# Optimization experiments

Hardware: AMD Instinct MI355X
Metric: run time of the kernel (lower is better)

The kernel has to match this reference:

```python
import jax, jax.numpy as jnp
import numpy as np

B, T, D = 8, 512, 1024
H, DQK, DV = 16, 128, 128  # n_heads, d_qk = emb_dim//h_qk, d_v = emb_dim//h_v


def setup_inputs() -> dict:
    key = jax.random.key(0)
    ks = jax.random.split(key, 8)
    s = 0.02
    return {
        "X": jax.random.normal(ks[0], (B, T, D), jnp.float32),
        "pos_enc_k": jax.random.normal(ks[1], (T, T, DQK), jnp.float32) * s,
        "pos_enc_v": jax.random.normal(ks[2], (T, T, DV), jnp.float32) * s,
        "Wq": jax.random.normal(ks[3], (D, H * DQK), jnp.float32) * s,
        "bq": jnp.zeros((H * DQK,), jnp.float32),
        "Wk": jax.random.normal(ks[4], (D, H * DQK), jnp.float32) * s,
        "bk": jnp.zeros((H * DQK,), jnp.float32),
        "Wv": jax.random.normal(ks[5], (D, H * DV), jnp.float32) * s,
        "bv": jnp.zeros((H * DV,), jnp.float32),
        "Wp": jax.random.normal(ks[6], (H * DV, D), jnp.float32) * s,
        "bp": jnp.zeros((D,), jnp.float32),
    }


def reference(X, pos_enc_k, pos_enc_v, Wq, bq, Wk, bk, Wv, bv, Wp, bp):
    b, t, d = X.shape
    # projections -> (b, h, t, dhead)
    Q = (X @ Wq + bq).reshape(b, t, H, DQK).transpose(0, 2, 1, 3)
    K = (X @ Wk + bk).reshape(b, t, H, DQK).transpose(0, 2, 1, 3)
    V = (X @ Wv + bv).reshape(b, t, H, DV).transpose(0, 2, 1, 3)
    # content attention + relative-position key bias
    att = jnp.einsum("bhqd,bhkd->bhqk", Q, K)
    att = att + jnp.einsum("bhqd,qkd->bhqk", Q, pos_enc_k)
    att = att / jnp.sqrt(jnp.asarray(DQK, X.dtype))
    # causal mask (do_mask=True)
    causal = jnp.tril(jnp.ones((t, t), bool))
    att = jnp.where(causal[None, None], att, jnp.asarray(-jnp.inf, att.dtype))
    att = jax.nn.softmax(att, axis=-1)
    # values + relative-position value correction
    y = jnp.einsum("bhqk,bhkd->bhqd", att, V)
    y = y + jnp.einsum("bhqk,qkd->bhqd", att, pos_enc_v)
    y = y.transpose(0, 2, 1, 3).reshape(b, t, H * DV)
    return y @ Wp + bp
```

## Files before the change

kernel.cpp:

```cpp
#include <hip/hip_runtime.h>
#include <stdint.h>

#define B_  8
#define T_  512
#define D_  1024
#define H_  16
#define DH  128
#define BH  128
#define ND  2048
#define BT  4096

typedef __attribute__((ext_vector_type(8))) short          short8;
typedef __attribute__((ext_vector_type(8))) __bf16         bf16x8;
typedef __attribute__((ext_vector_type(4))) float          f32x4;
typedef __attribute__((ext_vector_type(4))) unsigned short ushort4v;

static __device__ __forceinline__ unsigned short f2bf(float f) {
  unsigned u = __builtin_bit_cast(unsigned, f);
  u += 0x7FFFu + ((u >> 16) & 1u);
  return (unsigned short)(u >> 16);
}
static __device__ __forceinline__ float bf2f(unsigned short h) {
  unsigned u = ((unsigned)h) << 16;
  return __builtin_bit_cast(float, u);
}
static __device__ __forceinline__ f32x4 mfma16(short8 a, short8 b, f32x4 c) {
  return __builtin_amdgcn_mfma_f32_16x16x32_bf16(
      __builtin_bit_cast(bf16x8, a), __builtin_bit_cast(bf16x8, b), c, 0, 0, 0);
}
static __device__ __forceinline__ void gload16(const unsigned short* g, unsigned short* l) {
  __builtin_amdgcn_global_load_lds(
      (const __attribute__((address_space(1))) void*)g,
      (__attribute__((address_space(3))) void*)l, 16, 0, 0);
}

template <int ROWS, int COLS>
static __device__ __forceinline__ void stage_gl2(unsigned short* lds,
                                                 const unsigned short* __restrict__ src,
                                                 long stride, int tid) {
  constexpr int CPR = COLS / 8;
#pragma unroll
  for (int it = 0; it < ROWS * COLS / 8 / 256; ++it) {
    int chunk = tid + it * 256;
    int r = chunk / CPR, c8 = (chunk % CPR) * 8;
    gload16(src + (long)r * stride + c8, lds + chunk * 8);
  }
}

template <int MR, int NR, int LDA, int LDB, int KD>
static __device__ __forceinline__ void mfma_blk(const unsigned short* As,
                                                const unsigned short* Bs,
                                                int a0, int b0, int lrow, int lk8,
                                                f32x4 (*acc)[NR]) {
#pragma unroll
  for (int ks = 0; ks < KD; ks += 32) {
    short8 a[MR], b[NR];
#pragma unroll
    for (int i = 0; i < MR; ++i) a[i] = *(const short8*)&As[(a0 + i * 16 + lrow) * LDA + ks + lk8];
#pragma unroll
    for (int j = 0; j < NR; ++j) b[j] = *(const short8*)&Bs[(b0 + j * 16 + lrow) * LDB + ks + lk8];
#pragma unroll
    for (int i = 0; i < MR; ++i)
#pragma unroll
      for (int j = 0; j < NR; ++j) acc[i][j] = mfma16(a[i], b[j], acc[i][j]);
  }
}

#define IDS4                             \
  const int tid  = threadIdx.x;          \
  const int lane = tid & 63;             \
  const int wid  = tid >> 6;             \
  const int lrow = lane & 15;            \
  const int lk8  = (lane >> 4) * 8;      \
  const int lr4  = (lane >> 4) * 4;      \
  const int wm = wid >> 1, wn = wid & 1;

#define LTS 132
#define LTQ 68

__global__ __launch_bounds__(256) void k_cvt(const float* __restrict__ in,
                                             unsigned short* __restrict__ outp, int n4) {
  int i = blockIdx.x * 256 + threadIdx.x;
  if (i >= n4) return;
  f32x4 v = ((const f32x4*)in)[i];
  ushort4v o;
  o.x = f2bf(v.x); o.y = f2bf(v.y); o.z = f2bf(v.z); o.w = f2bf(v.w);
  ((ushort4v*)outp)[i] = o;
}

__global__ __launch_bounds__(256) void k_transcvt(const float* __restrict__ in,
                                                  unsigned short* __restrict__ outp,
                                                  int R, int C) {
  __shared__ float tile[32][33];
  int c0 = blockIdx.x * 32, r0 = blockIdx.y * 32;
  int tx = threadIdx.x & 31, ty = threadIdx.x >> 5;
#pragma unroll
  for (int i = 0; i < 32; i += 8)
    tile[ty + i][tx] = in[(long)(r0 + ty + i) * C + (c0 + tx)];
  __syncthreads();
#pragma unroll
  for (int i = 0; i < 32; i += 8)
    outp[(long)(c0 + ty + i) * R + (r0 + tx)] = f2bf(tile[tx][ty + i]);
}

__global__ __launch_bounds__(256) void k_vtrans(const unsigned short* __restrict__ vin,
                                                unsigned short* __restrict__ vout) {
  __shared__ unsigned short tile[32][33];
  int bh = blockIdx.z;
  int t0 = blockIdx.x * 32, d0 = blockIdx.y * 32;
  int tx = threadIdx.x & 31, ty = threadIdx.x >> 5;
#pragma unroll
  for (int i = 0; i < 32; i += 8)
    tile[ty + i][tx] = vin[((long)bh * T_ + t0 + ty + i) * DH + (d0 + tx)];
  __syncthreads();
#pragma unroll
  for (int i = 0; i < 32; i += 8)
    vout[((long)bh * DH + (d0 + ty + i)) * T_ + (t0 + tx)] = tile[tx][ty + i];
}

__global__ __launch_bounds__(512, 1) void k_proj8(const unsigned short* __restrict__ Xb,
                                                  const unsigned short* __restrict__ WT,
                                                  const float* __restrict__ bq,
                                                  const float* __restrict__ bk,
                                                  const float* __restrict__ bv,
                                                  unsigned short* __restrict__ Qb,
                                                  unsigned short* __restrict__ Kb,
                                                  unsigned short* __restrict__ Vb) {
  __shared__ unsigned short lds[3 * 24576];
  const int tid  = threadIdx.x;
  const int lane = tid & 63;
  const int wid  = tid >> 6;
  const int wm   = wid >> 2;
  const int wn   = wid & 3;
  const int lrow = lane & 15;
  const int lr4  = (lane >> 4) * 4;

  const int flat = blockIdx.x, xcd = flat & 7, local = flat >> 3;
  const int mt = (xcd & 1) * 16 + (local & 15);
  const int nt = (xcd >> 1) * 6 + (local >> 4);
  const int m0 = mt * 128, n0 = nt * 256;

  const unsigned short* Asrc = Xb + (long)m0 * D_;
  const unsigned short* Bsrc = WT + (long)n0 * D_;

  auto stageA = [&](int t) {
    unsigned short* base = lds + (t % 3) * 24576;
    const unsigned short* as = Asrc + t * 64;
#pragma unroll
    for (int it = 0; it < 2; ++it) {
      int n = tid + it * 512;
      int r = n >> 3, c = (n & 7) ^ (r & 7);
      gload16(as + (long)r * D_ + c * 8, base + n * 8);
    }
  };
  auto stageB = [&](int t) {
    unsigned short* base = lds + (t % 3) * 24576 + 8192;
    const unsigned short* bs = Bsrc + t * 64;
#pragma unroll
    for (int it = 0; it < 4; ++it) {
      int n = tid + it * 512;
      int r = n >> 3, c = (n & 7) ^ (r & 7);
      gload16(bs + (long)r * D_ + c * 8, base + 8192 + n * 8 - 8192);
    }
  };

  stageA(0); stageB(0);
  stageA(1); stageB(1);

  f32x4 acc[4][4] = {};
  for (int t = 0; t < 16; ++t) {
    if (t < 15) asm volatile("s_waitcnt vmcnt(6)" ::: "memory");
    else        asm volatile("s_waitcnt vmcnt(0)" ::: "memory");
    __builtin_amdgcn_sched_barrier(0);
    __builtin_amdgcn_s_barrier();
    __builtin_amdgcn_sched_barrier(0);
    const unsigned short* At = lds + (t % 3) * 24576;
    const unsigned short* Bt = At + 8192;
    {
      short8 a[4], b[4];
#pragma unroll
      for (int i = 0; i < 4; ++i) {
        int ra = wm * 64 + i * 16 + lrow;
        int c = (lane >> 4) ^ (ra & 7);
        a[i] = *(const short8*)&At[ra * 64 + c * 8];
      }
#pragma unroll
      for (int j = 0; j < 4; ++j) {
        int rb = wn * 64 + j * 16 + lrow;
        int c = (lane >> 4) ^ (rb & 7);
        b[j] = *(const short8*)&Bt[rb * 64 + c * 8];
      }
      if (t < 14) stageA(t + 2);
      __builtin_amdgcn_s_setprio(1);
#pragma unroll
      for (int i = 0; i < 4; ++i)
#pragma unroll
        for (int j = 0; j < 4; ++j)
          acc[i][j] = mfma16(a[i], b[j], acc[i][j]);
      __builtin_amdgcn_s_setprio(0);
    }
    __builtin_amdgcn_s_barrier();
    __builtin_amdgcn_sched_barrier(0);
    {
      short8 a[4], b[4];
#pragma unroll
      for (int i = 0; i < 4; ++i) {
        int ra = wm * 64 + i * 16 + lrow;
        int c = (4 + (lane >> 4)) ^ (ra & 7);
        a[i] = *(const short8*)&At[ra * 64 + c * 8];
      }
#pragma unroll
      for (int j = 0; j < 4; ++j) {
        int rb = wn * 64 + j * 16 + lrow;
        int c = (4 + (lane >> 4)) ^ (rb & 7);
        b[j] = *(const short8*)&Bt[rb * 64 + c * 8];
      }
      if (t < 14) stageB(t + 2);
      __builtin_amdgcn_s_setprio(1);
#pragma unroll
      for (int i = 0; i < 4; ++i)
#pragma unroll
        for (int j = 0; j < 4; ++j)
          acc[i][j] = mfma16(a[i], b[j], acc[i][j]);
      __builtin_amdgcn_s_setprio(0);
    }
  }

  const int nb = n0 >> 11;
  const float* biasp = nb == 0 ? bq : (nb == 1 ? bk : bv);
  unsigned short* dst = nb == 0 ? Qb : (nb == 1 ? Kb : Vb);
#pragma unroll
  for (int i = 0; i < 4; ++i)
#pragma unroll
    for (int j = 0; j < 4; ++j) {
      int c = (n0 & 2047) + wn * 64 + j * 16 + lrow;
      int h = c >> 7, dd = c & 127;
      float bias = biasp[c];
#pragma unroll
      for (int r = 0; r < 4; ++r) {
        int m = m0 + wm * 64 + i * 16 + lr4 + r;
        int bb = m >> 9, tt = m & (T_ - 1);
        dst[((long)(bb * H_ + h) * T_ + tt) * DH + dd] = f2bf(acc[i][j][r] + bias);
      }
    }
}

__global__ __launch_bounds__(256) void k_posk(const unsigned short* __restrict__ Qb,
                                              const float* __restrict__ Pk,
                                              unsigned short* __restrict__ att) {
  const int bid = blockIdx.x;
  const int q = (bid & 1) ? (T_ - 1 - (bid >> 1)) : (bid >> 1);
  const int ktiles = (q >> 6) + 1;
  __shared__ unsigned short As[128 * 128];
  __shared__ unsigned short Bs[2][64 * 136];
  IDS4
  stage_gl2<128, 128>(As, Qb + (long)q * DH, (long)T_ * DH, tid);
  f32x4 pv[8];
  const float* psrc = Pk + (long)q * T_ * DH;
  auto loadPk = [&](int kt) {
#pragma unroll
    for (int it = 0; it < 8; ++it) {
      int chunk = tid + it * 256;
      int r = chunk >> 5, c4 = (chunk & 31) * 4;
      pv[it] = *(const f32x4*)(psrc + (long)(kt * 64 + r) * DH + c4);
    }
  };
  auto writeB = [&](int buf) {
#pragma unroll
    for (int it = 0; it < 8; ++it) {
      int chunk = tid + it * 256;
      int r = chunk >> 5, c4 = (chunk & 31) * 4;
      ushort4v o;
      o.x = f2bf(pv[it].x); o.y = f2bf(pv[it].y); o.z = f2bf(pv[it].z); o.w = f2bf(pv[it].w);
      *(ushort4v*)&Bs[buf][r * 136 + c4] = o;
    }
  };
  loadPk(0);
  asm volatile("s_waitcnt vmcnt(0)" ::: "memory");
  writeB(0);
  asm volatile("s_waitcnt lgkmcnt(0)" ::: "memory");
  __builtin_amdgcn_s_barrier();
  for (int kt = 0; kt < ktiles; ++kt) {
    const bool pre = (kt + 1 < ktiles);
    if (pre) loadPk(kt + 1);
    f32x4 acc[4][2] = {};
    mfma_blk<4, 2, 128, 136, 128>(As, Bs[kt & 1], wm * 64, wn * 32, lrow, lk8, acc);
    if (pre) {
      asm volatile("s_waitcnt vmcnt(0)" ::: "memory");
      writeB((kt + 1) & 1);
    }
#pragma unroll
    for (int i = 0; i < 4; ++i)
#pragma unroll
      for (int j = 0; j < 2; ++j) {
        int k = kt * 64 + wn * 32 + j * 16 + lrow;
#pragma unroll
        for (int r = 0; r < 4; ++r) {
          int bh = wm * 64 + i * 16 + lr4 + r;
          att[((long)q * BH + bh) * T_ + k] = f2bf(acc[i][j][r]);
        }
      }
    asm volatile("s_waitcnt lgkmcnt(0)" ::: "memory");
    __builtin_amdgcn_s_barrier();
  }
}

__global__ __launch_bounds__(256) void k_qkv(const unsigned short* __restrict__ Qb,
                                             const unsigned short* __restrict__ Kb,
                                             const unsigned short* __restrict__ Vt,
                                             unsigned short* __restrict__ att,
                                             float* __restrict__ Sinv,
                                             unsigned short* __restrict__ Ybb) {
  const int bh = blockIdx.x & 127, pr = blockIdx.x >> 7;
  __shared__ unsigned short Qs[64 * 128], Ks[64 * 128], Vs[128 * 64];
  __shared__ unsigned short Ps[64 * 72];
  __shared__ float lt[64 * LTQ];
  __shared__ float sInv[64];
  const int tid = threadIdx.x;
  const int lane = tid & 63, wid = tid >> 6;
  const int wm = wid >> 1, wn = wid & 1;
  const int lrow = lane & 15, lk8 = (lane >> 4) * 8, lr4 = (lane >> 4) * 4;
  const int row = tid >> 2, c0 = (tid & 3) * 16;
  const float scale = 0.08838834764831845f;
  const int b = bh >> 4, h = bh & 15;

  for (int pass = 0; pass < 2; ++pass) {
    const int qt = pass ? 7 - pr : pr;
    const int q0 = qt * 64, ktiles = qt + 1;
    const int qabs = q0 + row;
    unsigned short* arow = att + ((long)qabs * BH + bh) * T_;
    {
      const unsigned short* src = Qb + ((long)bh * T_ + q0) * DH;
#pragma unroll
      for (int it = 0; it < 4; ++it) {
        int n = tid + it * 256;
        int r = n >> 4, c = (n & 15) ^ (r & 7);
        gload16(src + (long)r * DH + c * 8, Qs + n * 8);
      }
    }
    float ssum = 0.f;
    f32x4 accv[2][4] = {};
    for (int kt = 0; kt < ktiles; ++kt) {
      const unsigned short* ksrc = Kb + ((long)bh * T_ + kt * 64) * DH;
#pragma unroll
      for (int it = 0; it < 4; ++it) {
        int n = tid + it * 256;
        int r = n >> 4, c = (n & 15) ^ (r & 7);
        gload16(ksrc + (long)r * DH + c * 8, Ks + n * 8);
      }
      const unsigned short* vsrc = Vt + (long)bh * DH * T_ + kt * 64;
#pragma unroll
      for (int it = 0; it < 4; ++it) {
        int n = tid + it * 256;
        int r = n >> 3, c = (n & 7) ^ (r & 7);
        gload16(vsrc + (long)r * T_ + c * 8, Vs + n * 8);
      }
      short8 pb0 = *(const short8*)(arow + kt * 64 + c0);
      short8 pb1 = *(const short8*)(arow + kt * 64 + c0 + 8);
      __syncthreads();
      f32x4 acc[2][2] = {};
#pragma unroll
      for (int ks = 0; ks < 4; ++ks) {
        short8 aq[2], bk2[2];
#pragma unroll
        for (int i = 0; i < 2; ++i) {
          int ra = wm * 32 + i * 16 + lrow;
          int c = (ks * 4 + (lane >> 4)) ^ (ra & 7);
          aq[i] = *(const short8*)&Qs[ra * 128 + c * 8];
        }
#pragma unroll
        for (int j = 0; j < 2; ++j) {
          int rb = wn * 32 + j * 16 + lrow;
          int c = (ks * 4 + (lane >> 4)) ^ (rb & 7);
          bk2[j] = *(const short8*)&Ks[rb * 128 + c * 8];
        }
#pragma unroll
        for (int i = 0; i < 2; ++i)
#pragma unroll
          for (int j = 0; j < 2; ++j)
            acc[i][j] = mfma16(aq[i], bk2[j], acc[i][j]);
      }
#pragma unroll
      for (int i = 0; i < 2; ++i)
#pragma unroll
        for (int j = 0; j < 2; ++j)
#pragma unroll
          for (int r = 0; r < 4; ++r)
            lt[(wm * 32 + i * 16 + lr4 + r) * LTQ + wn * 32 + j * 16 + lrow] = acc[i][j][r];
      __syncthreads();
      short8 o0, o1;
#pragma unroll
      for (int jj = 0; jj < 8; ++jj) {
        int k = kt * 64 + c0 + jj;
        float e0 = (k <= qabs)
                   ? __expf((lt[row * LTQ + c0 + jj] + bf2f((unsigned short)pb0[jj])) * scale) : 0.f;
        float e1 = (k + 8 <= qabs)
                   ? __expf((lt[row * LTQ + c0 + 8 + jj] + bf2f((unsigned short)pb1[jj])) * scale) : 0.f;
        o0[jj] = (short)f2bf(e0);
        o1[jj] = (short)f2bf(e1);
        ssum += e0 + e1;
      }
      *(short8*)(arow + kt * 64 + c0) = o0;
      *(short8*)(arow + kt * 64 + c0 + 8) = o1;
      *(short8*)&Ps[row * 72 + c0] = o0;
      *(short8*)&Ps[row * 72 + c0 + 8] = o1;
      __syncthreads();
#pragma unroll
      for (int ks = 0; ks < 2; ++ks) {
        short8 ap[2], bv2[4];
#pragma unroll
        for (int i = 0; i < 2; ++i) {
          int ra = wm * 32 + i * 16 + lrow;
          ap[i] = *(const short8*)&Ps[ra * 72 + ks * 32 + lk8];
        }
#pragma unroll
        for (int j = 0; j < 4; ++j) {
          int rb = wn * 64 + j * 16 + lrow;
          int c = ((ks * 4) + (lane >> 4)) ^ (rb & 7);
          bv2[j] = *(const short8*)&Vs[rb * 64 + c * 8];
        }
#pragma unroll
        for (int i = 0; i < 2; ++i)
#pragma unroll
          for (int j = 0; j < 4; ++j)
            accv[i][j] = mfma16(ap[i], bv2[j], accv[i][j]);
      }
      __syncthreads();
    }
    ssum += __shfl_xor(ssum, 1, 64);
    ssum += __shfl_xor(ssum, 2, 64);
    float si = 1.f / ssum;
    if ((tid & 3) == 0) { sInv[row] = si; Sinv[(long)qabs * BH + bh] = si; }
    __syncthreads();
#pragma unroll
    for (int i = 0; i < 2; ++i) {
      float sc2[4];
#pragma unroll
      for (int r = 0; r < 4; ++r) sc2[r] = sInv[wm * 32 + i * 16 + lr4 + r];
#pragma unroll
      for (int j = 0; j < 4; ++j) {
        int d = wn * 64 + j * 16 + lrow;
#pragma unroll
        for (int r = 0; r < 4; ++r) {
          int q = q0 + wm * 32 + i * 16 + lr4 + r;
          Ybb[(long)(b * T_ + q) * ND + h * DH + d] = f2bf(accv[i][j][r] * sc2[r]);
        }
      }
    }
    __syncthreads();
  }
}

__global__ __launch_bounds__(256) void k_posv(const unsigned short* __restrict__ P,
                                              const float* __restrict__ Pv,
                                              const float* __restrict__ Sinv,
                                              unsigned short* __restrict__ Ybb) {
  const int bid = blockIdx.x;
  const int q = (bid & 1) ? (T_ - 1 - (bid >> 1)) : (bid >> 1);
  const int ktiles = (q >> 6) + 1;
  __shared__ unsigned short As[128 * 64];
  __shared__ unsigned short Bs[2][128 * 72];
  __shared__ float lt[64 * LTQ];
  IDS4
  f32x4 pv[8];
  const float* psrc = Pv + (long)q * T_ * DH;
  auto loadPv = [&](int kt) {
#pragma unroll
    for (int it = 0; it < 8; ++it) {
      int chunk = tid + it * 256;
      int d4 = (chunk & 3) * 4 + ((chunk >> 6) & 7) * 16;
      int k  = ((chunk >> 2) & 15) + ((chunk >> 9) & 3) * 16;
      pv[it] = *(const f32x4*)(psrc + (long)(kt * 64 + k) * DH + d4);
    }
  };
  auto writeB = [&](int buf) {
#pragma unroll
    for (int it = 0; it < 8; ++it) {
      int chunk = tid + it * 256;
      int d4 = (chunk & 3) * 4 + ((chunk >> 6) & 7) * 16;
      int k  = ((chunk >> 2) & 15) + ((chunk >> 9) & 3) * 16;
      Bs[buf][(d4 + 0) * 72 + k] = f2bf(pv[it].x);
      Bs[buf][(d4 + 1) * 72 + k] = f2bf(pv[it].y);
      Bs[buf][(d4 + 2) * 72 + k] = f2bf(pv[it].z);
      Bs[buf][(d4 + 3) * 72 + k] = f2bf(pv[it].w);
    }
  };
  loadPv(0);
  asm volatile("s_waitcnt vmcnt(0)" ::: "memory");
  writeB(0);
  asm volatile("s_waitcnt lgkmcnt(0)" ::: "memory");
  __builtin_amdgcn_s_barrier();
  f32x4 acc[4][4] = {};
  for (int kt = 0; kt < ktiles; ++kt) {
    const bool pre = (kt + 1 < ktiles);
    stage_gl2<128, 64>(As, P + (long)q * BH * T_ + kt * 64, T_, tid);
    if (pre) loadPv(kt + 1);
    if (pre) asm volatile("s_waitcnt vmcnt(8)" ::: "memory");
    else     asm volatile("s_waitcnt vmcnt(0)" ::: "memory");
    __builtin_amdgcn_s_barrier();
    mfma_blk<4, 4, 64, 72, 64>(As, Bs[kt & 1], wm * 64, wn * 64, lrow, lk8, acc);
    if (pre) {
      asm volatile("s_waitcnt vmcnt(0)" ::: "memory");
      writeB((kt + 1) & 1);
    }
    asm volatile("s_waitcnt lgkmcnt(0)" ::: "memory");
    __builtin_amdgcn_s_barrier();
  }
  const int row = tid >> 2, c0 = (tid & 3) * 16;
#pragma unroll
  for (int hb = 0; hb < 2; ++hb)
#pragma unroll
    for (int hd = 0; hd < 2; ++hd) {
      int bh = hb * 64 + row;
      long idx = ((long)((bh >> 4) * T_ + q)) * ND + (bh & 15) * DH + hd * 64 + c0;
      short8 y0 = *(const short8*)&Ybb[idx];
      short8 y1 = *(const short8*)&Ybb[idx + 8];
      float sc = Sinv[(long)q * BH + bh];
      if (wm == hb && wn == hd) {
#pragma unroll
        for (int i = 0; i < 4; ++i)
#pragma unroll
          for (int j = 0; j < 4; ++j)
#pragma unroll
            for (int r = 0; r < 4; ++r)
              lt[(i * 16 + lr4 + r) * LTQ + j * 16 + lrow] = acc[i][j][r];
      }
      __syncthreads();
      short8 o0, o1;
#pragma unroll
      for (int jj = 0; jj < 8; ++jj) {
        o0[jj] = (short)f2bf(lt[row * LTQ + c0 + jj] * sc + bf2f((unsigned short)y0[jj]));
        o1[jj] = (short)f2bf(lt[row * LTQ + c0 + 8 + jj] * sc + bf2f((unsigned short)y1[jj]));
      }
      *(short8*)&Ybb[idx] = o0;
      *(short8*)&Ybb[idx + 8] = o1;
      __syncthreads();
    }
}

__global__ __launch_bounds__(256) void k_oproj(const unsigned short* __restrict__ Ybb,
                                               const unsigned short* __restrict__ WpT,
                                               const float* __restrict__ bp,
                                               float* __restrict__ outp) {
  __shared__ unsigned short As[128 * 64], Bs[128 * 64];
  IDS4
  const int m0 = blockIdx.y * 128, n0 = blockIdx.x * 128;
  f32x4 acc[4][4] = {};
  for (int kk = 0; kk < ND; kk += 64) {
    stage_gl2<128, 64>(As, Ybb + (long)m0 * ND + kk, ND, tid);
    stage_gl2<128, 64>(Bs, WpT + (long)n0 * ND + kk, ND, tid);
    __syncthreads();
    mfma_blk<4, 4, 64, 64, 64>(As, Bs, wm * 64, wn * 64, lrow, lk8, acc);
    __syncthreads();
  }
  float* lt = (float*)As;
  const int row = tid >> 4, c8 = (tid & 15) * 8;
  f32x4 b0 = *(const f32x4*)(bp + n0 + c8);
  f32x4 b1 = *(const f32x4*)(bp + n0 + c8 + 4);
#pragma unroll
  for (int rr = 0; rr < 8; ++rr) {
    if (wm == (rr >> 2)) {
      const int ii = rr & 3;
#pragma unroll
      for (int j = 0; j < 4; ++j)
#pragma unroll
        for (int r = 0; r < 4; ++r)
          lt[(lr4 + r) * LTS + wn * 64 + j * 16 + lrow] = acc[ii][j][r];
    }
    __syncthreads();
    f32x4 v0 = *(const f32x4*)&lt[row * LTS + c8];
    f32x4 v1 = *(const f32x4*)&lt[row * LTS + c8 + 4];
    int m = m0 + rr * 16 + row;
    v0.x += b0.x; v0.y += b0.y; v0.z += b0.z; v0.w += b0.w;
    v1.x += b1.x; v1.y += b1.y; v1.z += b1.z; v1.w += b1.w;
    *(f32x4*)&outp[(long)m * D_ + n0 + c8] = v0;
    *(f32x4*)&outp[(long)m * D_ + n0 + c8 + 4] = v1;
    __syncthreads();
  }
}

extern "C" void kernel_launch(void* const* d_in, const int* in_sizes, int n_in,
                              void* d_out, int out_size, void* d_ws, size_t ws_size,
                              hipStream_t stream) {
  const float* X  = (const float*)d_in[0];
  const float* Pk = (const float*)d_in[1];
  const float* Pv = (const float*)d_in[2];
  const float* Wq = (const float*)d_in[3];
  const float* bq = (const float*)d_in[4];
  const float* Wk = (const float*)d_in[5];
  const float* bk = (const float*)d_in[6];
  const float* Wv = (const float*)d_in[7];
  const float* bv = (const float*)d_in[8];
  const float* Wp = (const float*)d_in[9];
  const float* bp = (const float*)d_in[10];
  float* out = (float*)d_out;

  uint8_t* w = (uint8_t*)d_ws;
  unsigned short* Xb  = (unsigned short*)w; w += (size_t)BT * D_ * 2;
  unsigned short* WT  = (unsigned short*)w; w += (size_t)3 * ND * D_ * 2;
  unsigned short* WpT = (unsigned short*)w; w += (size_t)D_ * ND * 2;
  unsigned short* Qb  = (unsigned short*)w; w += (size_t)BH * T_ * DH * 2;
  unsigned short* Kb  = (unsigned short*)w; w += (size_t)BH * T_ * DH * 2;
  unsigned short* Vb  = (unsigned short*)w; w += (size_t)BH * T_ * DH * 2;
  unsigned short* Vt  = (unsigned short*)w; w += (size_t)BH * DH * T_ * 2;
  unsigned short* att = (unsigned short*)w; w += (size_t)T_ * BH * T_ * 2;
  unsigned short* Ybb = (unsigned short*)w; w += (size_t)BT * ND * 2;
  float*          Sinv= (float*)w;          w += (size_t)T_ * BH * 4;

  k_cvt<<<BT * D_ / 4 / 256, 256, 0, stream>>>(X, Xb, BT * D_ / 4);
  k_transcvt<<<dim3(ND / 32, D_ / 32), 256, 0, stream>>>(Wq, WT, D_, ND);
  k_transcvt<<<dim3(ND / 32, D_ / 32), 256, 0, stream>>>(Wk, WT + (size_t)ND * D_, D_, ND);
  k_transcvt<<<dim3(ND / 32, D_ / 32), 256, 0, stream>>>(Wv, WT + (size_t)2 * ND * D_, D_, ND);
  k_transcvt<<<dim3(D_ / 32, ND / 32), 256, 0, stream>>>(Wp, WpT, ND, D_);
  k_proj8<<<768, 512, 0, stream>>>(Xb, WT, bq, bk, bv, Qb, Kb, Vb);
  k_vtrans<<<dim3(T_ / 32, DH / 32, BH), 256, 0, stream>>>(Vb, Vt);
  k_posk<<<T_, 256, 0, stream>>>(Qb, Pk, att);
  k_qkv<<<512, 256, 0, stream>>>(Qb, Kb, Vt, att, Sinv, Ybb);
  k_posv<<<T_, 256, 0, stream>>>(att, Pv, Sinv, Ybb);
  k_oproj<<<dim3(D_ / 128, BT / 128), 256, 0, stream>>>(Ybb, WpT, bp, out);
}
```

Measured before the change: 254.1 us.

## Merge prep conversion kernels and restructure QKV GEMM into four-phase pipeline

Folds the X conversion and the four weight transpose-convert launches into one k_prep kernel, cutting five launches down to one. Separately, the k_proj8 main loop is reorganized into four phases per k-tile, each computing a 2x2 sub-block of MFMAs. Global loads for the next stage are spread as A, B1 and B2 across the phases, with the vmcnt wait moved to the last phase. The finer interleaving is meant to overlap loads with compute better, at the cost of more barriers per iteration.

After: 254.8 us. No clear change (+0.3%).

```diff
diff --git a/kernel.cpp b/kernel.cpp
--- a/kernel.cpp
+++ b/kernel.cpp
@@ -78,21 +78,39 @@
 #define LTS 132
 #define LTQ 68
 
-__global__ __launch_bounds__(256) void k_cvt(const float* __restrict__ in,
-                                             unsigned short* __restrict__ outp, int n4) {
-  int i = blockIdx.x * 256 + threadIdx.x;
-  if (i >= n4) return;
-  f32x4 v = ((const f32x4*)in)[i];
-  ushort4v o;
-  o.x = f2bf(v.x); o.y = f2bf(v.y); o.z = f2bf(v.z); o.w = f2bf(v.w);
-  ((ushort4v*)outp)[i] = o;
-}
-
-__global__ __launch_bounds__(256) void k_transcvt(const float* __restrict__ in,
-                                                  unsigned short* __restrict__ outp,
-                                                  int R, int C) {
+__global__ __launch_bounds__(256) void k_prep(const float* __restrict__ X,
+                                              unsigned short* __restrict__ Xb,
+                                              const float* __restrict__ Wq,
+                                              const float* __restrict__ Wk,
+                                              const float* __restrict__ Wv,
+                                              const float* __restrict__ Wp,
+                                              unsigned short* __restrict__ WT,
+                                              unsigned short* __restrict__ WpT) {
   __shared__ float tile[32][33];
-  int c0 = blockIdx.x * 32, r0 = blockIdx.y * 32;
+  int bid = blockIdx.x;
+  if (bid < 4096) {
+    int i = bid * 256 + threadIdx.x;
+    f32x4 v = ((const f32x4*)X)[i];
+    ushort4v o;
+    o.x = f2bf(v.x); o.y = f2bf(v.y); o.z = f2bf(v.z); o.w = f2bf(v.w);
+    ((ushort4v*)Xb)[i] = o;
+    return;
+  }
+  bid -= 4096;
+  const int which = bid >> 11;
+  const int local = bid & 2047;
+  const float* in;
+  unsigned short* outp;
+  int R, C, bx, by;
+  if (which < 3) {
+    in = which == 0 ? Wq : (which == 1 ? Wk : Wv);
+    outp = WT + (size_t)which * ND * D_;
+    R = D_; C = ND; bx = local & 63; by = local >> 6;
+  } else {
+    in = Wp; outp = WpT;
+    R = ND; C = D_; bx = local & 31; by = local >> 5;
+  }
+  int c0 = bx * 32, r0 = by * 32;
   int tx = threadIdx.x & 31, ty = threadIdx.x >> 5;
 #pragma unroll
   for (int i = 0; i < 32; i += 8)
@@ -153,76 +171,83 @@
       gload16(as + (long)r * D_ + c * 8, base + n * 8);
     }
   };
-  auto stageB = [&](int t) {
+  auto stageB1 = [&](int t) {
     unsigned short* base = lds + (t % 3) * 24576 + 8192;
     const unsigned short* bs = Bsrc + t * 64;
 #pragma unroll
-    for (int it = 0; it < 4; ++it) {
+    for (int it = 0; it < 2; ++it) {
       int n = tid + it * 512;
       int r = n >> 3, c = (n & 7) ^ (r & 7);
-      gload16(bs + (long)r * D_ + c * 8, base + 8192 + n * 8 - 8192);
+      gload16(bs + (long)r * D_ + c * 8, base + n * 8);
     }
   };
-
-  stageA(0); stageB(0);
-  stageA(1); stageB(1);
+  auto stageB2 = [&](int t) {
+    unsigned short* base = lds + (t % 3) * 24576 + 8192;
+    const unsigned short* bs = Bsrc + t * 64;
+#pragma unroll
+    for (int it = 2; it < 4; ++it) {
+      int n = tid + it * 512;
+      int r = n >> 3, c = (n & 7) ^ (r & 7);
+      gload16(bs + (long)r * D_ + c * 8, base + n * 8);
+    }
+  };
+
+  stageA(0); stageB1(0); stageB2(0);
+  stageA(1); stageB1(1); stageB2(1);
+  asm volatile("s_waitcnt vmcnt(6)" ::: "memory");
+  __builtin_amdgcn_sched_barrier(0);
+  __builtin_amdgcn_s_barrier();
 
   f32x4 acc[4][4] = {};
   for (int t = 0; t < 16; ++t) {
-    if (t < 15) asm volatile("s_waitcnt vmcnt(6)" ::: "memory");
-    else        asm volatile("s_waitcnt vmcnt(0)" ::: "memory");
-    __builtin_amdgcn_sched_barrier(0);
-    __builtin_amdgcn_s_barrier();
-    __builtin_amdgcn_sched_barrier(0);
     const unsigned short* At = lds + (t % 3) * 24576;
     const unsigned short* Bt = At + 8192;
-    {
-      short8 a[4], b[4];
-#pragma unroll
-      for (int i = 0; i < 4; ++i) {
-        int ra = wm * 64 + i * 16 + lrow;
-        int c = (lane >> 4) ^ (ra & 7);
-        a[i] = *(const short8*)&At[ra * 64 + c * 8];
-      }
-#pragma unroll
-      for (int j = 0; j < 4; ++j) {
-        int rb = wn * 64 + j * 16 + lrow;
-        int c = (lane >> 4) ^ (rb & 7);
-        b[j] = *(const short8*)&Bt[rb * 64 + c * 8];
-      }
-      if (t < 14) stageA(t + 2);
+#pragma unroll
+    for (int ph = 0; ph < 4; ++ph) {
+      const int mh = ph >> 1, nh = ph & 1;
+      short8 a[2][2], b[2][2];
+#pragma unroll
+      for (int i = 0; i < 2; ++i) {
+        int ra = wm * 64 + mh * 32 + i * 16 + lrow;
+#pragma unroll
+        for (int ks = 0; ks < 2; ++ks) {
+          int c = (ks * 4 + (lane >> 4)) ^ (ra & 7);
+          a[i][ks] = *(const short8*)&At[ra * 64 + c * 8];
+        }
+      }
+#pragma unroll
+      for (int j = 0; j < 2; ++j) {
+        int rb = wn * 64 + nh * 32 + j * 16 + lrow;
+#pragma unroll
+        for (int ks = 0; ks < 2; ++ks) {
+          int c = (ks * 4 + (lane >> 4)) ^ (rb & 7);
+          b[j][ks] = *(const short8*)&Bt[rb * 64 + c * 8];
+        }
+      }
+      if (t < 14) {
+        if (ph == 0) stageA(t + 2);
+        else if (ph == 1) stageB1(t + 2);
+        else if (ph == 2) stageB2(t + 2);
+      }
+      if (ph == 3) {
+        if (t < 14) asm volatile("s_waitcnt vmcnt(6)" ::: "memory");
+        else        asm volatile("s_waitcnt vmcnt(0)" ::: "memory");
+        __builtin_amdgcn_sched_barrier(0);
+      }
+      __builtin_amdgcn_s_barrier();
+      asm volatile("s_waitcnt lgkmcnt(0)" ::: "memory");
+      __builtin_amdgcn_sched_barrier(0);
       __builtin_amdgcn_s_setprio(1);
 #pragma unroll
-      for (int i = 0; i < 4; ++i)
-#pragma unroll
-        for (int j = 0; j < 4; ++j)
-          acc[i][j] = mfma16(a[i], b[j], acc[i][j]);
+      for (int ks = 0; ks < 2; ++ks)
+#pragma unroll
+        for (int i = 0; i < 2; ++i)
+#pragma unroll
+          for (int j = 0; j < 2; ++j)
+            acc[mh * 2 + i][nh * 2 + j] =
+                mfma16(a[i][ks], b[j][ks], acc[mh * 2 + i][nh * 2 + j]);
       __builtin_amdgcn_s_setprio(0);
-    }
-    __builtin_amdgcn_s_barrier();
-    __builtin_amdgcn_sched_barrier(0);
-    {
-      short8 a[4], b[4];
-#pragma unroll
-      for (int i = 0; i < 4; ++i) {
-        int ra = wm * 64 + i * 16 + lrow;
-        int c = (4 + (lane >> 4)) ^ (ra & 7);
-        a[i] = *(const short8*)&At[ra * 64 + c * 8];
-      }
-#pragma unroll
-      for (int j = 0; j < 4; ++j) {
-        int rb = wn * 64 + j * 16 + lrow;
-        int c = (4 + (lane >> 4)) ^ (rb & 7);
-        b[j] = *(const short8*)&Bt[rb * 64 + c * 8];
-      }
-      if (t < 14) stageB(t + 2);
-      __builtin_amdgcn_s_setprio(1);
-#pragma unroll
-      for (int i = 0; i < 4; ++i)
-#pragma unroll
-        for (int j = 0; j < 4; ++j)
-          acc[i][j] = mfma16(a[i], b[j], acc[i][j]);
-      __builtin_amdgcn_s_setprio(0);
+      __builtin_amdgcn_s_barrier();
     }
   }
 
@@ -607,11 +632,7 @@
   unsigned short* Ybb = (unsigned short*)w; w += (size_t)BT * ND * 2;
   float*          Sinv= (float*)w;          w += (size_t)T_ * BH * 4;
 
-  k_cvt<<<BT * D_ / 4 / 256, 256, 0, stream>>>(X, Xb, BT * D_ / 4);
-  k_transcvt<<<dim3(ND / 32, D_ / 32), 256, 0, stream>>>(Wq, WT, D_, ND);
-  k_transcvt<<<dim3(ND / 32, D_ / 32), 256, 0, stream>>>(Wk, WT + (size_t)ND * D_, D_, ND);
-  k_transcvt<<<dim3(ND / 32, D_ / 32), 256, 0, stream>>>(Wv, WT + (size_t)2 * ND * D_, D_, ND);
-  k_transcvt<<<dim3(D_ / 32, ND / 32), 256, 0, stream>>>(Wp, WpT, ND, D_);
+  k_prep<<<12288, 256, 0, stream>>>(X, Xb, Wq, Wk, Wv, Wp, WT, WpT);
   k_proj8<<<768, 512, 0, stream>>>(Xb, WT, bq, bk, bv, Qb, Kb, Vb);
   k_vtrans<<<dim3(T_ / 32, DH / 32, BH), 256, 0, stream>>>(Vb, Vt);
   k_posk<<<T_, 256, 0, stream>>>(Qb, Pk, att);
```
